# Performance work log

Measured on AMD Instinct MI355X. Metric: run time of the kernel, lower is better.

Reference implementation:

```python
import jax, jax.numpy as jnp
import numpy as np

D_MODEL = 1024

def setup_inputs() -> dict:
    key = jax.random.key(0)
    ks = jax.random.split(key, 7)
    x = jax.random.normal(ks[0], (4, 4096, D_MODEL), dtype=jnp.float32)
    s = 1.0 / np.sqrt(D_MODEL)
    Wq = jax.random.uniform(ks[1], (D_MODEL, D_MODEL), jnp.float32, -s, s)
    bq = jax.random.uniform(ks[2], (D_MODEL,), jnp.float32, -s, s)
    Wk = jax.random.uniform(ks[3], (D_MODEL, D_MODEL), jnp.float32, -s, s)
    bk = jax.random.uniform(ks[4], (D_MODEL,), jnp.float32, -s, s)
    Wv = jax.random.uniform(ks[5], (D_MODEL, D_MODEL), jnp.float32, -s, s)
    bv = jax.random.uniform(ks[6], (D_MODEL,), jnp.float32, -s, s)
    return {"x": x, "Wq": Wq, "bq": bq, "Wk": Wk, "bk": bk, "Wv": Wv, "bv": bv}

def reference(x, Wq, bq, Wk, bk, Wv, bv):
    # Q, K, V: [b, s, d]
    Q = jnp.einsum('bsd,ed->bse', x, Wq) + bq
    K = jnp.einsum('bsd,ed->bse', x, Wk) + bk
    V = jnp.einsum('bsd,ed->bse', x, Wv) + bv
    scale = 1.0 / jnp.sqrt(jnp.asarray(D_MODEL, dtype=x.dtype))
    scores = jnp.einsum('bqd,bkd->bqk', Q, K) * scale  # [b, s, s]
    attn = jax.nn.softmax(scores, axis=-1)
    return jnp.einsum('bqk,bkd->bqd', attn, V)
```

## Files before the change

### kernel.cpp

```cpp
#include <hip/hip_runtime.h>
#include <stdint.h>
#include <stddef.h>

#define DM 1024
#define SEQ 4096
#define NB 4
#define NTOK (NB*SEQ)

typedef __attribute__((ext_vector_type(8))) short s16x8;
typedef __attribute__((ext_vector_type(4))) float f32x4;

__device__ __forceinline__ unsigned short f2bf(float f) {
  unsigned int u = __float_as_uint(f);
  u += 0x7FFFu + ((u >> 16) & 1u);
  return (unsigned short)(u >> 16);
}

__device__ __forceinline__ f32x4 mfma16(s16x8 a, s16x8 b, f32x4 c) {
  return __builtin_amdgcn_mfma_f32_16x16x32_bf16(a, b, c, 0, 0, 0);
}

__device__ __forceinline__ void gload16(const void* g, void* l) {
  __builtin_amdgcn_global_load_lds((const __attribute__((address_space(1))) unsigned int*)g,
                                   (__attribute__((address_space(3))) unsigned int*)l, 16, 0, 0);
}

__global__ void k_conv(const float* __restrict__ s, unsigned short* __restrict__ d, int n8) {
  int i = blockIdx.x * blockDim.x + threadIdx.x;
  int st = gridDim.x * blockDim.x;
  for (; i < n8; i += st) {
    const f32x4* sp = (const f32x4*)s + (size_t)i * 2;
    f32x4 a = sp[0], b = sp[1];
    s16x8 o;
    o[0] = (short)f2bf(a[0]); o[1] = (short)f2bf(a[1]);
    o[2] = (short)f2bf(a[2]); o[3] = (short)f2bf(a[3]);
    o[4] = (short)f2bf(b[0]); o[5] = (short)f2bf(b[1]);
    o[6] = (short)f2bf(b[2]); o[7] = (short)f2bf(b[3]);
    *((s16x8*)d + i) = o;
  }
}

template<int KDIM, int EPI>
__device__ __forceinline__ void gemm_core(
    const unsigned short* __restrict__ A, const unsigned short* __restrict__ B,
    void* __restrict__ outp, int ldc, const float* __restrict__ bias, float scale,
    int mbase, int nbase)
{
  __shared__ unsigned short lds[2][2][128 * 64];
  const int tid = threadIdx.x, lane = tid & 63, wid = tid >> 6;
  const int wr = wid >> 1, wc = wid & 1;
  const int l7 = lane & 7, l3 = lane >> 3, l15 = lane & 15, lg = lane >> 4;
  const int scol = ((l7 ^ l3) << 3);

  f32x4 acc[4][4];
  #pragma unroll
  for (int m = 0; m < 4; m++)
    #pragma unroll
    for (int n = 0; n < 4; n++) { acc[m][n][0]=0.f; acc[m][n][1]=0.f; acc[m][n][2]=0.f; acc[m][n][3]=0.f; }

  auto stage = [&](int buf, int kt) {
    const int kb_ = kt * 64;
    #pragma unroll
    for (int j = 0; j < 8; j++) {
      int i = wid * 8 + j;
      if (i < 16) {
        const unsigned short* src = A + (size_t)(mbase + i * 8 + l3) * KDIM + kb_ + scol;
        gload16(src, &lds[buf][0][i * 512]);
      } else {
        int ib = i - 16;
        const unsigned short* src = B + (size_t)(nbase + ib * 8 + l3) * KDIM + kb_ + scol;
        gload16(src, &lds[buf][1][ib * 512]);
      }
    }
  };

  auto compute = [&](int buf) {
    s16x8 af[4][2], bf[4][2];
    #pragma unroll
    for (int m = 0; m < 4; m++)
      #pragma unroll
      for (int k2 = 0; k2 < 2; k2++) {
        int row = wr * 64 + m * 16 + l15;
        int off = (row * 128 + k2 * 64 + lg * 16) ^ ((row & 7) << 4);
        af[m][k2] = *(const s16x8*)((const char*)&lds[buf][0][0] + off);
      }
    #pragma unroll
    for (int n = 0; n < 4; n++)
      #pragma unroll
      for (int k2 = 0; k2 < 2; k2++) {
        int row = wc * 64 + n * 16 + l15;
        int off = (row * 128 + k2 * 64 + lg * 16) ^ ((row & 7) << 4);
        bf[n][k2] = *(const s16x8*)((const char*)&lds[buf][1][0] + off);
      }
    #pragma unroll
    for (int k2 = 0; k2 < 2; k2++)
      #pragma unroll
      for (int m = 0; m < 4; m++)
        #pragma unroll
        for (int n = 0; n < 4; n++)
          acc[m][n] = mfma16(af[m][k2], bf[n][k2], acc[m][n]);
  };

  stage(0, 0);
  __syncthreads();
  constexpr int NT = KDIM / 64;
  for (int kt = 0; kt < NT; kt++) {
    int cur = kt & 1;
    if (kt < NT - 1) stage(cur ^ 1, kt + 1);
    compute(cur);
    __syncthreads();
  }

  #pragma unroll
  for (int n = 0; n < 4; n++) {
    int col = nbase + wc * 64 + n * 16 + l15;
    float bb = (EPI == 0) ? bias[col] : 0.f;
    #pragma unroll
    for (int m = 0; m < 4; m++) {
      #pragma unroll
      for (int r = 0; r < 4; r++) {
        int row = mbase + wr * 64 + m * 16 + lg * 4 + r;
        float v = acc[m][n][r];
        if (EPI == 0) {
          ((unsigned short*)outp)[(size_t)row * ldc + col] = f2bf(v + bb);
        } else if (EPI == 1) {
          _Float16 h = (_Float16)(v * scale);
          ((unsigned short*)outp)[(size_t)row * ldc + col] = __builtin_bit_cast(unsigned short, h);
        } else {
          ((float*)outp)[(size_t)row * ldc + col] = v;
        }
      }
    }
  }
}

__global__ __launch_bounds__(256, 2) void k_qkv(
    const unsigned short* __restrict__ xb, const unsigned short* __restrict__ wb,
    const float* __restrict__ b0, const float* __restrict__ b1, const float* __restrict__ b2,
    unsigned short* __restrict__ qo, unsigned short* __restrict__ ko, unsigned short* __restrict__ vo)
{
  const int z = blockIdx.z;
  gemm_core<DM, 0>(xb, wb + (size_t)z * DM * DM,
                   (z == 0) ? qo : (z == 1) ? ko : vo, DM,
                   (z == 0) ? b0 : (z == 1) ? b1 : b2, 0.f,
                   blockIdx.y * 128, blockIdx.x * 128);
}

__global__ void k_transpose(const unsigned short* __restrict__ v, unsigned short* __restrict__ vt) {
  __shared__ unsigned short t[64][65];
  const int b = blockIdx.z;
  const int rbase = blockIdx.x * 64;
  const int cbase = blockIdx.y * 64;
  const unsigned short* vb = v + (size_t)b * SEQ * DM;
  unsigned short* vtb = vt + (size_t)b * DM * SEQ;
  const int tid = threadIdx.x;
  #pragma unroll
  for (int it = 0; it < 16; it++) {
    int idx = it * 256 + tid;
    int r = idx >> 6, c = idx & 63;
    t[r][c] = vb[(size_t)(rbase + r) * DM + cbase + c];
  }
  __syncthreads();
  #pragma unroll
  for (int it = 0; it < 16; it++) {
    int idx = it * 256 + tid;
    int oc = idx >> 6, ot = idx & 63;
    vtb[(size_t)(cbase + oc) * SEQ + rbase + ot] = t[ot][oc];
  }
}

__global__ __launch_bounds__(256, 2) void k_sgemm(
    const unsigned short* __restrict__ qb, const unsigned short* __restrict__ kb,
    unsigned short* __restrict__ sc0, unsigned short* __restrict__ sc1, int bb)
{
  const int z = blockIdx.z;
  gemm_core<DM, 1>(qb + (size_t)(bb + z) * SEQ * DM, kb + (size_t)(bb + z) * SEQ * DM,
                   z ? sc1 : sc0, SEQ, nullptr, 0.03125f,
                   blockIdx.y * 128, blockIdx.x * 128);
}

__global__ __launch_bounds__(256) void k_softmax(unsigned short* __restrict__ sc0,
                                                 unsigned short* __restrict__ sc1) {
  unsigned short* sc = blockIdx.z ? sc1 : sc0;
  const int row = blockIdx.x * 4 + (threadIdx.x >> 6);
  const int lane = threadIdx.x & 63;
  unsigned short* rp = sc + (size_t)row * SEQ + lane * 8;

  s16x8 v[8];
  #pragma unroll
  for (int j = 0; j < 8; j++) v[j] = *(const s16x8*)(rp + (size_t)j * 512);

  float f[64];
  float m = -1e30f;
  #pragma unroll
  for (int j = 0; j < 8; j++)
    #pragma unroll
    for (int t = 0; t < 8; t++) {
      float x = (float)__builtin_bit_cast(_Float16, (unsigned short)v[j][t]);
      f[j * 8 + t] = x;
      m = fmaxf(m, x);
    }
  m = fmaxf(m, __shfl_xor(m, 1));  m = fmaxf(m, __shfl_xor(m, 2));
  m = fmaxf(m, __shfl_xor(m, 4));  m = fmaxf(m, __shfl_xor(m, 8));
  m = fmaxf(m, __shfl_xor(m, 16)); m = fmaxf(m, __shfl_xor(m, 32));

  float s = 0.f;
  #pragma unroll
  for (int i = 0; i < 64; i++) { f[i] = __expf(f[i] - m); s += f[i]; }
  s += __shfl_xor(s, 1);  s += __shfl_xor(s, 2);  s += __shfl_xor(s, 4);
  s += __shfl_xor(s, 8);  s += __shfl_xor(s, 16); s += __shfl_xor(s, 32);
  float inv = 1.f / s;

  #pragma unroll
  for (int j = 0; j < 8; j++) {
    s16x8 o;
    #pragma unroll
    for (int t = 0; t < 8; t++) o[t] = (short)f2bf(f[j * 8 + t] * inv);
    *(s16x8*)(rp + (size_t)j * 512) = o;
  }
}

__global__ __launch_bounds__(256, 2) void k_pv(
    const unsigned short* __restrict__ sc0, const unsigned short* __restrict__ sc1,
    const unsigned short* __restrict__ vt, float* __restrict__ out, int bb)
{
  const int z = blockIdx.z;
  gemm_core<SEQ, 2>(z ? sc1 : sc0, vt + (size_t)(bb + z) * DM * SEQ,
                    out + (size_t)(bb + z) * SEQ * DM, DM, nullptr, 1.f,
                    blockIdx.y * 128, blockIdx.x * 128);
}

extern "C" void kernel_launch(void* const* d_in, const int* in_sizes, int n_in,
                              void* d_out, int out_size, void* d_ws, size_t ws_size,
                              hipStream_t stream) {
  const float* x  = (const float*)d_in[0];
  const float* Wq = (const float*)d_in[1];
  const float* bq = (const float*)d_in[2];
  const float* Wk = (const float*)d_in[3];
  const float* bk = (const float*)d_in[4];
  const float* Wv = (const float*)d_in[5];
  const float* bv = (const float*)d_in[6];
  float* out = (float*)d_out;
  char* ws = (char*)d_ws;

  unsigned short* xb = (unsigned short*)(ws);
  unsigned short* wb = (unsigned short*)(ws + 33554432);
  unsigned short* qb = (unsigned short*)(ws + 39845888);
  unsigned short* kb = (unsigned short*)(ws + 73400320);
  unsigned short* vb = (unsigned short*)(ws + 106954752);
  unsigned short* vt = (unsigned short*)(ws + 140509184);
  unsigned short* sc0 = xb;
  unsigned short* sc1 = vb;

  k_conv<<<4096, 256, 0, stream>>>(x, xb, NTOK * DM / 8);
  k_conv<<<512, 256, 0, stream>>>(Wq, wb, DM * DM / 8);
  k_conv<<<512, 256, 0, stream>>>(Wk, wb + DM * DM, DM * DM / 8);
  k_conv<<<512, 256, 0, stream>>>(Wv, wb + 2 * DM * DM, DM * DM / 8);

  k_qkv<<<dim3(8, 128, 3), 256, 0, stream>>>(xb, wb, bq, bk, bv, qb, kb, vb);
  k_transpose<<<dim3(64, 16, 4), 256, 0, stream>>>(vb, vt);

  for (int bb = 0; bb < NB; bb += 2) {
    k_sgemm<<<dim3(32, 32, 2), 256, 0, stream>>>(qb, kb, sc0, sc1, bb);
    k_softmax<<<dim3(1024, 1, 2), 256, 0, stream>>>(sc0, sc1);
    k_pv<<<dim3(8, 32, 2), 256, 0, stream>>>(sc0, sc1, vt, out, bb);
  }
}
```

Measured before the change: 537.3 us.

## Replace GEMM core with 8-wave triple-buffered pipelined kernel and larger tiles

The 4-wave double-buffered GEMM core is replaced by an 8-wave (512-thread) kernel. It uses 256x256 tiles for QKV and scores and 128x256 for PV, K-steps of 32, and a three-stage LDS ring. It overlaps loads with compute using explicit vmcnt waits, raw barriers, interleaved per-phase staging and setprio around the MFMA bursts. The aim is to hide global-load latency and raise MFMA utilisation through more reuse per tile, at the cost of more barriers per K-step and fewer blocks per grid.

```diff
diff --git a/kernel.cpp b/kernel.cpp
--- a/kernel.cpp
+++ b/kernel.cpp
@@ -23,6 +23,13 @@
 __device__ __forceinline__ void gload16(const void* g, void* l) {
   __builtin_amdgcn_global_load_lds((const __attribute__((address_space(1))) unsigned int*)g,
                                    (__attribute__((address_space(3))) unsigned int*)l, 16, 0, 0);
+}
+
+template<int N> __device__ __forceinline__ void vmcnt() {
+  asm volatile("s_waitcnt vmcnt(%0)" :: "n"(N) : "memory");
+}
+__device__ __forceinline__ void rawbar() {
+  asm volatile("s_barrier" ::: "memory");
 }
 
 __global__ void k_conv(const float* __restrict__ s, unsigned short* __restrict__ d, int n8) {
@@ -40,75 +47,111 @@
   }
 }
 
-template<int KDIM, int EPI>
-__device__ __forceinline__ void gemm_core(
+template<int KD, int BM, int EPI>
+__device__ __forceinline__ void gemm8p(
     const unsigned short* __restrict__ A, const unsigned short* __restrict__ B,
     void* __restrict__ outp, int ldc, const float* __restrict__ bias, float scale,
     int mbase, int nbase)
 {
-  __shared__ unsigned short lds[2][2][128 * 64];
+  constexpr int NT  = KD / 32;
+  constexpr int PH  = BM / 128;
+  constexpr int WR  = BM / 2;
+  constexpr int MR  = WR / 16;
+  constexpr int AL  = BM * 32;
+  constexpr int LJA = BM / 128;
+  constexpr int LPT = LJA + 2;
+
+  __shared__ unsigned short lA[3][AL];
+  __shared__ unsigned short lB[3][256 * 32];
+
   const int tid = threadIdx.x, lane = tid & 63, wid = tid >> 6;
-  const int wr = wid >> 1, wc = wid & 1;
-  const int l7 = lane & 7, l3 = lane >> 3, l15 = lane & 15, lg = lane >> 4;
-  const int scol = ((l7 ^ l3) << 3);
-
-  f32x4 acc[4][4];
-  #pragma unroll
-  for (int m = 0; m < 4; m++)
+  const int wr = wid >> 2, wc = wid & 3;
+  const int l15 = lane & 15, lg = lane >> 4;
+
+  int aSrc[LJA], bSrc[2];
+  #pragma unroll
+  for (int j = 0; j < LJA; j++) {
+    int s = j * 512 + wid * 64 + lane;
+    int row = s >> 2, k8 = (s & 3) ^ ((row >> 1) & 3);
+    aSrc[j] = (mbase + row) * KD + k8 * 8;
+  }
+  #pragma unroll
+  for (int j = 0; j < 2; j++) {
+    int s = j * 512 + wid * 64 + lane;
+    int row = s >> 2, k8 = (s & 3) ^ ((row >> 1) & 3);
+    bSrc[j] = (nbase + row) * KD + k8 * 8;
+  }
+
+  int aOff[MR], bOff[4];
+  #pragma unroll
+  for (int m = 0; m < MR; m++) {
+    int row = wr * WR + m * 16 + l15;
+    aOff[m] = row * 32 + ((lg ^ ((row >> 1) & 3)) * 8);
+  }
+  #pragma unroll
+  for (int n = 0; n < 4; n++) {
+    int row = wc * 64 + n * 16 + l15;
+    bOff[n] = row * 32 + ((lg ^ ((row >> 1) & 3)) * 8);
+  }
+
+  auto stA = [&](int c2, int kt, int j) {
+    gload16(A + (size_t)aSrc[j] + kt * 32, &lA[c2][(j * 512 + wid * 64) * 8]);
+  };
+  auto stB = [&](int c2, int kt, int j) {
+    gload16(B + (size_t)bSrc[j] + kt * 32, &lB[c2][(j * 512 + wid * 64) * 8]);
+  };
+
+  f32x4 acc[MR][4];
+  #pragma unroll
+  for (int m = 0; m < MR; m++)
     #pragma unroll
     for (int n = 0; n < 4; n++) { acc[m][n][0]=0.f; acc[m][n][1]=0.f; acc[m][n][2]=0.f; acc[m][n][3]=0.f; }
 
-  auto stage = [&](int buf, int kt) {
-    const int kb_ = kt * 64;
-    #pragma unroll
-    for (int j = 0; j < 8; j++) {
-      int i = wid * 8 + j;
-      if (i < 16) {
-        const unsigned short* src = A + (size_t)(mbase + i * 8 + l3) * KDIM + kb_ + scol;
-        gload16(src, &lds[buf][0][i * 512]);
-      } else {
-        int ib = i - 16;
-        const unsigned short* src = B + (size_t)(nbase + ib * 8 + l3) * KDIM + kb_ + scol;
-        gload16(src, &lds[buf][1][ib * 512]);
+  #pragma unroll
+  for (int j = 0; j < LJA; j++) stA(0, 0, j);
+  stB(0, 0, 0); stB(0, 0, 1);
+  #pragma unroll
+  for (int j = 0; j < LJA; j++) stA(1, 1, j);
+  stB(1, 1, 0); stB(1, 1, 1);
+  vmcnt<LPT>();
+  rawbar();
+
+  int cur = 0;
+  for (int t = 0; t < NT; t++) {
+    int c2 = cur + 2; if (c2 >= 3) c2 -= 3;
+    #pragma unroll
+    for (int ph = 0; ph < PH; ph++) {
+      s16x8 af[4], bf[4];
+      #pragma unroll
+      for (int i = 0; i < 4; i++)
+        af[i] = *(const s16x8*)(&lA[cur][0] + aOff[ph * 4 + i]);
+      #pragma unroll
+      for (int n = 0; n < 4; n++)
+        bf[n] = *(const s16x8*)(&lB[cur][0] + bOff[n]);
+
+      if (t + 2 < NT) {
+        if (PH == 2) {
+          if (ph == 0) { stA(c2, t + 2, 0); if (LJA > 1) stA(c2, t + 2, LJA - 1); }
+          else         { stB(c2, t + 2, 0); stB(c2, t + 2, 1); }
+        } else {
+          stA(c2, t + 2, 0); stB(c2, t + 2, 0); stB(c2, t + 2, 1);
+        }
       }
-    }
-  };
-
-  auto compute = [&](int buf) {
-    s16x8 af[4][2], bf[4][2];
-    #pragma unroll
-    for (int m = 0; m < 4; m++)
+      if (ph == PH - 1) {
+        if (t + 2 < NT)      vmcnt<LPT>();
+        else if (t + 1 < NT) vmcnt<0>();
+      }
+      rawbar();
+      __builtin_amdgcn_s_setprio(1);
       #pragma unroll
-      for (int k2 = 0; k2 < 2; k2++) {
-        int row = wr * 64 + m * 16 + l15;
-        int off = (row * 128 + k2 * 64 + lg * 16) ^ ((row & 7) << 4);
-        af[m][k2] = *(const s16x8*)((const char*)&lds[buf][0][0] + off);
-      }
-    #pragma unroll
-    for (int n = 0; n < 4; n++)
-      #pragma unroll
-      for (int k2 = 0; k2 < 2; k2++) {
-        int row = wc * 64 + n * 16 + l15;
-        int off = (row * 128 + k2 * 64 + lg * 16) ^ ((row & 7) << 4);
-        bf[n][k2] = *(const s16x8*)((const char*)&lds[buf][1][0] + off);
-      }
-    #pragma unroll
-    for (int k2 = 0; k2 < 2; k2++)
-      #pragma unroll
-      for (int m = 0; m < 4; m++)
+      for (int i = 0; i < 4; i++)
         #pragma unroll
         for (int n = 0; n < 4; n++)
-          acc[m][n] = mfma16(af[m][k2], bf[n][k2], acc[m][n]);
-  };
-
-  stage(0, 0);
-  __syncthreads();
-  constexpr int NT = KDIM / 64;
-  for (int kt = 0; kt < NT; kt++) {
-    int cur = kt & 1;
-    if (kt < NT - 1) stage(cur ^ 1, kt + 1);
-    compute(cur);
-    __syncthreads();
+          acc[ph * 4 + i][n] = mfma16(af[i], bf[n], acc[ph * 4 + i][n]);
+      __builtin_amdgcn_s_setprio(0);
+      rawbar();
+    }
+    cur++; if (cur >= 3) cur = 0;
   }
 
   #pragma unroll
@@ -116,10 +159,10 @@
     int col = nbase + wc * 64 + n * 16 + l15;
     float bb = (EPI == 0) ? bias[col] : 0.f;
     #pragma unroll
-    for (int m = 0; m < 4; m++) {
+    for (int m = 0; m < MR; m++) {
       #pragma unroll
       for (int r = 0; r < 4; r++) {
-        int row = mbase + wr * 64 + m * 16 + lg * 4 + r;
+        int row = mbase + wr * WR + m * 16 + lg * 4 + r;
         float v = acc[m][n][r];
         if (EPI == 0) {
           ((unsigned short*)outp)[(size_t)row * ldc + col] = f2bf(v + bb);
@@ -134,16 +177,16 @@
   }
 }
 
-__global__ __launch_bounds__(256, 2) void k_qkv(
+__global__ __launch_bounds__(512, 2) void k_qkv(
     const unsigned short* __restrict__ xb, const unsigned short* __restrict__ wb,
     const float* __restrict__ b0, const float* __restrict__ b1, const float* __restrict__ b2,
     unsigned short* __restrict__ qo, unsigned short* __restrict__ ko, unsigned short* __restrict__ vo)
 {
   const int z = blockIdx.z;
-  gemm_core<DM, 0>(xb, wb + (size_t)z * DM * DM,
-                   (z == 0) ? qo : (z == 1) ? ko : vo, DM,
-                   (z == 0) ? b0 : (z == 1) ? b1 : b2, 0.f,
-                   blockIdx.y * 128, blockIdx.x * 128);
+  gemm8p<DM, 256, 0>(xb, wb + (size_t)z * DM * DM,
+                     (z == 0) ? qo : (z == 1) ? ko : vo, DM,
+                     (z == 0) ? b0 : (z == 1) ? b1 : b2, 0.f,
+                     blockIdx.y * 256, blockIdx.x * 256);
 }
 
 __global__ void k_transpose(const unsigned short* __restrict__ v, unsigned short* __restrict__ vt) {
@@ -169,14 +212,14 @@
   }
 }
 
-__global__ __launch_bounds__(256, 2) void k_sgemm(
+__global__ __launch_bounds__(512, 2) void k_sgemm(
     const unsigned short* __restrict__ qb, const unsigned short* __restrict__ kb,
     unsigned short* __restrict__ sc0, unsigned short* __restrict__ sc1, int bb)
 {
   const int z = blockIdx.z;
-  gemm_core<DM, 1>(qb + (size_t)(bb + z) * SEQ * DM, kb + (size_t)(bb + z) * SEQ * DM,
-                   z ? sc1 : sc0, SEQ, nullptr, 0.03125f,
-                   blockIdx.y * 128, blockIdx.x * 128);
+  gemm8p<DM, 256, 1>(qb + (size_t)(bb + z) * SEQ * DM, kb + (size_t)(bb + z) * SEQ * DM,
+                     z ? sc1 : sc0, SEQ, nullptr, 0.03125f,
+                     blockIdx.y * 256, blockIdx.x * 256);
 }
 
 __global__ __launch_bounds__(256) void k_softmax(unsigned short* __restrict__ sc0,
@@ -220,14 +263,14 @@
   }
 }
 
-__global__ __launch_bounds__(256, 2) void k_pv(
+__global__ __launch_bounds__(512, 2) void k_pv(
     const unsigned short* __restrict__ sc0, const unsigned short* __restrict__ sc1,
     const unsigned short* __restrict__ vt, float* __restrict__ out, int bb)
 {
   const int z = blockIdx.z;
-  gemm_core<SEQ, 2>(z ? sc1 : sc0, vt + (size_t)(bb + z) * DM * SEQ,
-                    out + (size_t)(bb + z) * SEQ * DM, DM, nullptr, 1.f,
-                    blockIdx.y * 128, blockIdx.x * 128);
+  gemm8p<SEQ, 128, 2>(z ? sc1 : sc0, vt + (size_t)(bb + z) * DM * SEQ,
+                      out + (size_t)(bb + z) * SEQ * DM, DM, nullptr, 1.f,
+                      blockIdx.y * 128, blockIdx.x * 256);
 }
 
 extern "C" void kernel_launch(void* const* d_in, const int* in_sizes, int n_in,
@@ -257,12 +300,12 @@
   k_conv<<<512, 256, 0, stream>>>(Wk, wb + DM * DM, DM * DM / 8);
   k_conv<<<512, 256, 0, stream>>>(Wv, wb + 2 * DM * DM, DM * DM / 8);
 
-  k_qkv<<<dim3(8, 128, 3), 256, 0, stream>>>(xb, wb, bq, bk, bv, qb, kb, vb);
+  k_qkv<<<dim3(4, 64, 3), 512, 0, stream>>>(xb, wb, bq, bk, bv, qb, kb, vb);
   k_transpose<<<dim3(64, 16, 4), 256, 0, stream>>>(vb, vt);
 
   for (int bb = 0; bb < NB; bb += 2) {
-    k_sgemm<<<dim3(32, 32, 2), 256, 0, stream>>>(qb, kb, sc0, sc1, bb);
+    k_sgemm<<<dim3(16, 16, 2), 512, 0, stream>>>(qb, kb, sc0, sc1, bb);
     k_softmax<<<dim3(1024, 1, 2), 256, 0, stream>>>(sc0, sc1);
-    k_pv<<<dim3(8, 32, 2), 256, 0, stream>>>(sc0, sc1, vt, out, bb);
-  }
-}
+    k_pv<<<dim3(4, 32, 2), 512, 0, stream>>>(sc0, sc1, vt, out, bb);
+  }
+}
```

Result: slower. 598.3 us (+11.3%).

## Add XCD-aware block swizzle, smaller K tile for QKV/score GEMMs, higher occupancy

Applied to the files above, without the earlier changes.

Adds a block-index remap that gives each of the 8 XCDs a contiguous range of tiles, so neighbouring tiles share that XCD's L2. The GEMM core is now templated on the K tile size. The QKV and score GEMMs use BK=32, which halves LDS per block and allows launch_bounds of 4 blocks per CU, with a matching swizzle pattern for loads. Higher occupancy may raise register pressure or cause spills, and the smaller K tile means twice as many barriers per K loop.

```diff
diff --git a/kernel.cpp b/kernel.cpp
--- a/kernel.cpp
+++ b/kernel.cpp
@@ -23,6 +23,14 @@
 __device__ __forceinline__ void gload16(const void* g, void* l) {
   __builtin_amdgcn_global_load_lds((const __attribute__((address_space(1))) unsigned int*)g,
                                    (__attribute__((address_space(3))) unsigned int*)l, 16, 0, 0);
+}
+
+__device__ __forceinline__ void xcd_swz(int gx, int gy, int& x, int& y, int& z) {
+  int nwg = gx * gy * gridDim.z;
+  int bid = blockIdx.x + gx * (blockIdx.y + gy * blockIdx.z);
+  int cpx = nwg >> 3;
+  int wg = (bid & 7) * cpx + (bid >> 3);
+  x = wg % gx; int t = wg / gx; y = t % gy; z = t / gy;
 }
 
 __global__ void k_conv(const float* __restrict__ s, unsigned short* __restrict__ d, int n8) {
@@ -40,17 +48,21 @@
   }
 }
 
-template<int KDIM, int EPI>
+template<int KD, int BK, int EPI>
 __device__ __forceinline__ void gemm_core(
     const unsigned short* __restrict__ A, const unsigned short* __restrict__ B,
     void* __restrict__ outp, int ldc, const float* __restrict__ bias, float scale,
     int mbase, int nbase)
 {
-  __shared__ unsigned short lds[2][2][128 * 64];
+  constexpr int NT     = KD / BK;
+  constexpr int SLOTS  = BK / 8;
+  constexpr int SMASK  = SLOTS - 1;
+  constexpr int PASSES = 128 * SLOTS / 256;
+
+  __shared__ unsigned short lds[2][2][128 * BK];
   const int tid = threadIdx.x, lane = tid & 63, wid = tid >> 6;
   const int wr = wid >> 1, wc = wid & 1;
-  const int l7 = lane & 7, l3 = lane >> 3, l15 = lane & 15, lg = lane >> 4;
-  const int scol = ((l7 ^ l3) << 3);
+  const int l15 = lane & 15, lg = lane >> 4;
 
   f32x4 acc[4][4];
   #pragma unroll
@@ -58,52 +70,50 @@
     #pragma unroll
     for (int n = 0; n < 4; n++) { acc[m][n][0]=0.f; acc[m][n][1]=0.f; acc[m][n][2]=0.f; acc[m][n][3]=0.f; }
 
+  auto rswz = [](int row) -> int { return (BK == 64) ? (row & 7) : ((row >> 1) & 3); };
+
   auto stage = [&](int buf, int kt) {
-    const int kb_ = kt * 64;
-    #pragma unroll
-    for (int j = 0; j < 8; j++) {
-      int i = wid * 8 + j;
-      if (i < 16) {
-        const unsigned short* src = A + (size_t)(mbase + i * 8 + l3) * KDIM + kb_ + scol;
-        gload16(src, &lds[buf][0][i * 512]);
-      } else {
-        int ib = i - 16;
-        const unsigned short* src = B + (size_t)(nbase + ib * 8 + l3) * KDIM + kb_ + scol;
-        gload16(src, &lds[buf][1][ib * 512]);
+    const int kb_ = kt * BK;
+    #pragma unroll
+    for (int p = 0; p < PASSES; p++) {
+      int s = p * 256 + tid;
+      int row = s / SLOTS, sl = (s & SMASK) ^ rswz(row);
+      gload16(A + (size_t)(mbase + row) * KD + kb_ + sl * 8, &lds[buf][0][s * 8]);
+    }
+    #pragma unroll
+    for (int p = 0; p < PASSES; p++) {
+      int s = p * 256 + tid;
+      int row = s / SLOTS, sl = (s & SMASK) ^ rswz(row);
+      gload16(B + (size_t)(nbase + row) * KD + kb_ + sl * 8, &lds[buf][1][s * 8]);
+    }
+  };
+
+  auto compute = [&](int buf) {
+    #pragma unroll
+    for (int k2 = 0; k2 < BK / 32; k2++) {
+      s16x8 af[4], bf[4];
+      #pragma unroll
+      for (int m = 0; m < 4; m++) {
+        int row = wr * 64 + m * 16 + l15;
+        int sl = (k2 * 4 + lg) ^ rswz(row);
+        af[m] = *(const s16x8*)(&lds[buf][0][0] + row * BK + sl * 8);
       }
-    }
-  };
-
-  auto compute = [&](int buf) {
-    s16x8 af[4][2], bf[4][2];
-    #pragma unroll
-    for (int m = 0; m < 4; m++)
-      #pragma unroll
-      for (int k2 = 0; k2 < 2; k2++) {
-        int row = wr * 64 + m * 16 + l15;
-        int off = (row * 128 + k2 * 64 + lg * 16) ^ ((row & 7) << 4);
-        af[m][k2] = *(const s16x8*)((const char*)&lds[buf][0][0] + off);
+      #pragma unroll
+      for (int n = 0; n < 4; n++) {
+        int row = wc * 64 + n * 16 + l15;
+        int sl = (k2 * 4 + lg) ^ rswz(row);
+        bf[n] = *(const s16x8*)(&lds[buf][1][0] + row * BK + sl * 8);
       }
-    #pragma unroll
-    for (int n = 0; n < 4; n++)
-      #pragma unroll
-      for (int k2 = 0; k2 < 2; k2++) {
-        int row = wc * 64 + n * 16 + l15;
-        int off = (row * 128 + k2 * 64 + lg * 16) ^ ((row & 7) << 4);
-        bf[n][k2] = *(const s16x8*)((const char*)&lds[buf][1][0] + off);
-      }
-    #pragma unroll
-    for (int k2 = 0; k2 < 2; k2++)
       #pragma unroll
       for (int m = 0; m < 4; m++)
         #pragma unroll
         for (int n = 0; n < 4; n++)
-          acc[m][n] = mfma16(af[m][k2], bf[n][k2], acc[m][n]);
+          acc[m][n] = mfma16(af[m], bf[n], acc[m][n]);
+    }
   };
 
   stage(0, 0);
   __syncthreads();
-  constexpr int NT = KDIM / 64;
   for (int kt = 0; kt < NT; kt++) {
     int cur = kt & 1;
     if (kt < NT - 1) stage(cur ^ 1, kt + 1);
@@ -134,16 +144,17 @@
   }
 }
 
-__global__ __launch_bounds__(256, 2) void k_qkv(
+__global__ __launch_bounds__(256, 4) void k_qkv(
     const unsigned short* __restrict__ xb, const unsigned short* __restrict__ wb,
     const float* __restrict__ b0, const float* __restrict__ b1, const float* __restrict__ b2,
     unsigned short* __restrict__ qo, unsigned short* __restrict__ ko, unsigned short* __restrict__ vo)
 {
-  const int z = blockIdx.z;
-  gemm_core<DM, 0>(xb, wb + (size_t)z * DM * DM,
-                   (z == 0) ? qo : (z == 1) ? ko : vo, DM,
-                   (z == 0) ? b0 : (z == 1) ? b1 : b2, 0.f,
-                   blockIdx.y * 128, blockIdx.x * 128);
+  int x, y, z;
+  xcd_swz(8, 128, x, y, z);
+  gemm_core<DM, 32, 0>(xb, wb + (size_t)z * DM * DM,
+                       (z == 0) ? qo : (z == 1) ? ko : vo, DM,
+                       (z == 0) ? b0 : (z == 1) ? b1 : b2, 0.f,
+                       y * 128, x * 128);
 }
 
 __global__ void k_transpose(const unsigned short* __restrict__ v, unsigned short* __restrict__ vt) {
@@ -169,14 +180,15 @@
   }
 }
 
-__global__ __launch_bounds__(256, 2) void k_sgemm(
+__global__ __launch_bounds__(256, 4) void k_sgemm(
     const unsigned short* __restrict__ qb, const unsigned short* __restrict__ kb,
     unsigned short* __restrict__ sc0, unsigned short* __restrict__ sc1, int bb)
 {
-  const int z = blockIdx.z;
-  gemm_core<DM, 1>(qb + (size_t)(bb + z) * SEQ * DM, kb + (size_t)(bb + z) * SEQ * DM,
-                   z ? sc1 : sc0, SEQ, nullptr, 0.03125f,
-                   blockIdx.y * 128, blockIdx.x * 128);
+  int x, y, z;
+  xcd_swz(32, 32, x, y, z);
+  gemm_core<DM, 32, 1>(qb + (size_t)(bb + z) * SEQ * DM, kb + (size_t)(bb + z) * SEQ * DM,
+                       z ? sc1 : sc0, SEQ, nullptr, 0.03125f,
+                       y * 128, x * 128);
 }
 
 __global__ __launch_bounds__(256) void k_softmax(unsigned short* __restrict__ sc0,
@@ -224,10 +236,11 @@
     const unsigned short* __restrict__ sc0, const unsigned short* __restrict__ sc1,
     const unsigned short* __restrict__ vt, float* __restrict__ out, int bb)
 {
-  const int z = blockIdx.z;
-  gemm_core<SEQ, 2>(z ? sc1 : sc0, vt + (size_t)(bb + z) * DM * SEQ,
-                    out + (size_t)(bb + z) * SEQ * DM, DM, nullptr, 1.f,
-                    blockIdx.y * 128, blockIdx.x * 128);
+  int x, y, z;
+  xcd_swz(8, 32, x, y, z);
+  gemm_core<SEQ, 64, 2>(z ? sc1 : sc0, vt + (size_t)(bb + z) * DM * SEQ,
+                        out + (size_t)(bb + z) * SEQ * DM, DM, nullptr, 1.f,
+                        y * 128, x * 128);
 }
 
 extern "C" void kernel_launch(void* const* d_in, const int* in_sizes, int n_in,
```

New measurement: 506.2 us. 5.8% less time.
